# Performance work log

Hardware: AMD Instinct MI355X
Metric: run time of the kernel (lower is better)

## Reference

```python
import jax, jax.numpy as jnp
from jax import lax
import numpy as np

GAMMA, WARP = 0.01, 134.4          # SoftDTW(gamma=0.01, warp=134.4)
INF, BIG = 100000.0, 1e9           # INF from kl_loss_sdtw; BIG ~ math.inf boundary
KL_A, KL_FWD_A, GEN_A, GEN_E2E_A, FEAT_A, DUR_A, MEL_A = 1.0, 1.0, 1.0, 1.0, 1.0, 1.0, 45.0


def soft_dtw(D):
    """Soft-DTW with warp penalty. D: [B, N, M] -> R[:, N, M].
    R[i,j] = D[i-1,j-1] + softmin_gamma(R[i-1,j-1], R[i-1,j]+warp, R[i,j-1]+warp)."""
    B, N, M = D.shape
    row0 = jnp.full((B, M + 1), BIG, D.dtype).at[:, 0].set(0.0)  # R[0, :]

    def row_step(prev_row, d_row):                 # prev_row: [B, M+1], d_row: [B, M]
        left0 = jnp.full((B,), BIG, D.dtype)       # R[i, 0]

        def col_step(r_left, inp):
            d, r_diag, r_up = inp                  # each [B]
            r0 = -r_diag / GAMMA
            r1 = -(r_up + WARP) / GAMMA
            r2 = -(r_left + WARP) / GAMMA
            rmax = jnp.maximum(jnp.maximum(r0, r1), r2)
            smin = -GAMMA * (jnp.log(jnp.exp(r0 - rmax) + jnp.exp(r1 - rmax) + jnp.exp(r2 - rmax)) + rmax)
            r = d + smin
            return r, r

        xs = (d_row.T, prev_row[:, :-1].T, prev_row[:, 1:].T)   # scan over j=1..M
        _, vals = lax.scan(col_step, left0, xs)                 # [M, B]
        new_row = jnp.concatenate([left0[:, None], vals.T], axis=1)
        return new_row, None

    last, _ = lax.scan(row_step, row0, jnp.swapaxes(D, 0, 1))   # scan over i=1..N
    return last[:, M]


def sdtw_kl_matrix(z, logs_q, m, logs_p):
    """kl[b,i,j] = sum_h logs_p - logs_q - 0.5 + 0.5*(z-m)^2*exp(-2 logs_p).
    m, logs_p: [b,h,tp]; z, logs_q: [b,h,tq] -> [b,tp,tq] via 3 batched GEMMs."""
    h = m.shape[1]
    w = jnp.exp(-2.0 * logs_p)                                   # [b,h,tp]
    quad = (jnp.einsum('bhi,bhj->bij', w, z * z)
            - 2.0 * jnp.einsum('bhi,bhj->bij', w * m, z)
            + jnp.sum(w * m * m, axis=1)[:, :, None])
    return (jnp.sum(logs_p, axis=1)[:, :, None]
            - jnp.sum(logs_q, axis=1)[:, None, :]
            - 0.5 * h + 0.5 * quad)


def kl_loss_sdtw(z, logs_q, m, logs_p, p_mask, q_mask):
    kl = sdtw_kl_matrix(z, logs_q, m, logs_p)
    kl = jnp.pad(kl, ((0, 0), (0, 1), (0, 1)))
    pm = jnp.pad(p_mask, ((0, 0), (0, 1)))
    qm = jnp.pad(q_mask, ((0, 0), (0, 1)))
    pb = pm[:, :, None].astype(bool)
    qb = qm[:, None, :].astype(bool)
    kl = jnp.where(pb ^ qb, INF, kl)
    kl = jnp.where((~pb) & (~qb), 0.0, kl)
    return jnp.sum(soft_dtw(kl)) / jnp.sum(pm)


def _forward(mel_slice, mel_slice_hat, scores_disc_fake, scores_disc_fake_e2e,
             feats_disc_real, feats_disc_fake, loss_duration, loss_duration_len,
             loss_pitch, z_p, m_p, logs_p, z_q, m_q, logs_q, p_mask, z_mask):
    # generator losses: sum over discriminators of mean((1-score)^2)
    loss_gen = jnp.sum(jnp.mean((1.0 - scores_disc_fake) ** 2, axis=(1, 2))) * GEN_A
    loss_gen_e2e = jnp.sum(jnp.mean((1.0 - scores_disc_fake_e2e) ** 2, axis=(1, 2))) * GEN_E2E_A
    # feature-matching loss (real feats detached)
    fr = lax.stop_gradient(feats_disc_real)
    loss_fm = jnp.sum(jnp.mean(jnp.abs(fr - feats_disc_fake), axis=(1, 2, 3))) * 2.0 * FEAT_A
    loss_mel = jnp.mean(jnp.abs(mel_slice - mel_slice_hat)) * MEL_A
    loss_dur = jnp.sum(loss_duration) * DUR_A
    loss_dur_len = jnp.log(loss_duration_len + 1e-6)
    zm = z_mask[:, 0, :]
    loss_kl = kl_loss_sdtw(z_p, logs_q, m_p, logs_p, p_mask, zm) * KL_A
    loss_kl_fwd = kl_loss_sdtw(z_q, logs_p, m_q, logs_q, zm, p_mask) * KL_FWD_A
    return (loss_gen + loss_gen_e2e + loss_fm + loss_mel + loss_dur
            + loss_dur_len + loss_kl + loss_kl_fwd)


def setup_inputs() -> dict:
    key = jax.random.key(0)
    ks = jax.random.split(key, 16)
    B, H, TP, TQ = 4, 192, 350, 400
    return {
        'mel_slice': jax.random.normal(ks[0], (B, 80, 128), jnp.float32),
        'mel_slice_hat': jax.random.normal(ks[1], (B, 80, 128), jnp.float32),
        'scores_disc_fake': jax.random.normal(ks[2], (6, B, 8192), jnp.float32),
        'scores_disc_fake_e2e': jax.random.normal(ks[3], (6, B, 8192), jnp.float32),
        'feats_disc_real': jax.random.normal(ks[4], (24, B, 128, 4096), jnp.float32),
        'feats_disc_fake': jax.random.normal(ks[5], (24, B, 128, 4096), jnp.float32),
        'loss_duration': jax.random.uniform(ks[6], (B, TP), jnp.float32) * 0.01,
        'loss_duration_len': jax.random.uniform(ks[7], (), jnp.float32) + 0.5,
        'loss_pitch': jax.random.uniform(ks[8], (B, TP), jnp.float32),
        'z_p': jax.random.normal(ks[9], (B, H, TQ), jnp.float32),
        'm_p': jax.random.normal(ks[10], (B, H, TP), jnp.float32),
        'logs_p': 0.1 * jax.random.normal(ks[11], (B, H, TP), jnp.float32),
        'z_q': jax.random.normal(ks[12], (B, H, TP), jnp.float32),
        'm_q': jax.random.normal(ks[13], (B, H, TQ), jnp.float32),
        'logs_q': 0.1 * jax.random.normal(ks[14], (B, H, TQ), jnp.float32),
        'p_mask': jnp.ones((B, TP), jnp.float32),
        'z_mask': jnp.ones((B, 1, TQ), jnp.float32),
    }


def reference(mel_slice, mel_slice_hat, scores_disc_fake, scores_disc_fake_e2e,
              feats_disc_real, feats_disc_fake, loss_duration, loss_duration_len,
              loss_pitch, z_p, m_p, logs_p, z_q, m_q, logs_q, p_mask, z_mask):
    return _forward(mel_slice, mel_slice_hat, scores_disc_fake, scores_disc_fake_e2e,
                    feats_disc_real, feats_disc_fake, loss_duration, loss_duration_len,
                    loss_pitch, z_p, m_p, logs_p, z_q, m_q, logs_q, p_mask, z_mask)
```

## Files before the change

### kernel.cpp

```cpp
#include <hip/hip_runtime.h>
#include <math.h>

#define GAMMA_ 0.01f
#define WARP_  134.4f
#define INFV   100000.0f
#define BIGV   1000000000.0f

#define B_  4
#define H_  192
#define TP_ 350
#define TQ_ 400

#define ACC_OFF 0
#define DTW_OFF 16
#define SLP_OFF 32
#define SLQ_OFF (SLP_OFF + B_*TP_)
#define KL1_OFF 3072
#define KL1_NCOL 401
#define KL1_PITCHT 352
#define KL2_OFF (KL1_OFF + B_*KL1_NCOL*KL1_PITCHT)
#define KL2_NCOL 351
#define KL2_PITCHT 408

#define RING_SLOTS 67
#define RING_PITCH 416

typedef float f4_t __attribute__((ext_vector_type(4)));

__device__ __forceinline__ unsigned pk2(float a, float b) {
    unsigned ua = __float_as_uint(a), ub = __float_as_uint(b);
    ua = (ua + 0x7FFFu + ((ua >> 16) & 1u)) >> 16;
    ub = (ub + 0x7FFFu + ((ub >> 16) & 1u)) & 0xFFFF0000u;
    return ua | ub;
}

__global__ void sl_kernel(const float* __restrict__ logs_p,
                          const float* __restrict__ logs_q,
                          float* __restrict__ ws) {
    int t = blockIdx.x * 256 + threadIdx.x;
    if (t < 32) ws[ACC_OFF + t] = 0.f;
    if (t < B_ * TP_) {
        int b = t / TP_, i = t % TP_;
        const float* p = logs_p + (size_t)b * H_ * TP_ + i;
        float s = 0.f;
        for (int h = 0; h < H_; ++h) s += p[(size_t)h * TP_];
        ws[SLP_OFF + t] = s;
    } else if (t < B_ * TP_ + B_ * TQ_) {
        int t2 = t - B_ * TP_;
        int b = t2 / TQ_, j = t2 % TQ_;
        const float* p = logs_q + (size_t)b * H_ * TQ_ + j;
        float s = 0.f;
        for (int h = 0; h < H_; ++h) s += p[(size_t)h * TQ_];
        ws[SLQ_OFF + t2] = s;
    }
}

__global__ void kl_kernel(const float* __restrict__ mp, const float* __restrict__ lsp,
                          const float* __restrict__ zp,
                          const float* __restrict__ mq, const float* __restrict__ lsq,
                          const float* __restrict__ zq,
                          const float* __restrict__ pmask, const float* __restrict__ zmask,
                          float* __restrict__ ws) {
    int which = blockIdx.z >> 2;
    int b     = blockIdx.z & 3;
    const float *mS, *lS, *zS, *SLrow, *SLcol, *rm, *cm; float* out; int R, C, pitchT;
    if (which == 0) { mS=mp; lS=lsp; zS=zp; SLrow=ws+SLP_OFF; SLcol=ws+SLQ_OFF;
                      rm=pmask + b*TP_; cm=zmask + b*TQ_;
                      out=ws+KL1_OFF + (size_t)b*KL1_NCOL*KL1_PITCHT;
                      R=TP_; C=TQ_; pitchT=KL1_PITCHT; }
    else            { mS=mq; lS=lsq; zS=zq; SLrow=ws+SLQ_OFF; SLcol=ws+SLP_OFF;
                      rm=zmask + b*TQ_; cm=pmask + b*TP_;
                      out=ws+KL2_OFF + (size_t)b*KL2_NCOL*KL2_PITCHT;
                      R=TQ_; C=TP_; pitchT=KL2_PITCHT; }
    int i0 = blockIdx.x * 32;
    int j0 = blockIdx.y * 32;
    if (i0 > R || j0 > C) return;
    __shared__ __align__(16) float wS [16][32];
    __shared__ __align__(16) float mSh[16][32];
    __shared__ __align__(16) float zSh[16][32];
    const float* mB = mS + (size_t)b * H_ * R;
    const float* lB = lS + (size_t)b * H_ * R;
    const float* zB = zS + (size_t)b * H_ * C;
    int tx = threadIdx.x, ty = threadIdx.y;
    int t  = ty * 16 + tx;
    float a00 = 0.f, a01 = 0.f, a10 = 0.f, a11 = 0.f;
    for (int h0 = 0; h0 < H_; h0 += 16) {
        for (int e = t; e < 512; e += 256) {
            int hh = e >> 5, cc = e & 31;
            int h = h0 + hh;
            int gi = i0 + cc, gj = j0 + cc;
            float wv = 0.f, mv = 0.f;
            if (gi < R) {
                wv = __expf(-2.f * lB[(size_t)h * R + gi]);
                mv = mB[(size_t)h * R + gi];
            }
            wS[hh][cc] = wv; mSh[hh][cc] = mv;
            zSh[hh][cc] = (gj < C) ? zB[(size_t)h * C + gj] : 0.f;
        }
        __syncthreads();
#pragma unroll
        for (int kk = 0; kk < 16; ++kk) {
            float2 wv = *(const float2*)&wS [kk][tx * 2];
            float2 mv = *(const float2*)&mSh[kk][tx * 2];
            float2 zv = *(const float2*)&zSh[kk][ty * 2];
            float d;
            d = zv.x - mv.x; a00 += wv.x * d * d;
            d = zv.x - mv.y; a01 += wv.y * d * d;
            d = zv.y - mv.x; a10 += wv.x * d * d;
            d = zv.y - mv.y; a11 += wv.y * d * d;
        }
        __syncthreads();
    }
    float accs[2][2] = {{a00, a01}, {a10, a11}};
    for (int jj = 0; jj < 2; ++jj)
        for (int ii = 0; ii < 2; ++ii) {
            int I = i0 + tx * 2 + ii, J = j0 + ty * 2 + jj;
            if (I <= R && J <= C) {
                bool pbI = (I < R) && (rm[I] != 0.f);
                bool qbJ = (J < C) && (cm[J] != 0.f);
                float v;
                if (pbI & qbJ)
                    v = SLrow[b * R + I] - SLcol[b * C + J] - 0.5f * H_ + 0.5f * accs[jj][ii];
                else
                    v = (pbI ^ qbJ) ? INFV : 0.f;
                out[(size_t)J * pitchT + I] = v;
            }
        }
}

#define SLD(q, r, cc, ii, vv) { int col_ = ((q) << 3) + (cc); \
    if ((vv) && col_ <= C_) r = *(const f4_t*)(klT + (size_t)col_ * pitchT + ((ii) << 2)); }
#define SST(q, r, cc, ii, vv) { int col_ = ((q) << 3) + (cc); \
    if ((vv) && col_ <= C_) { int s_ = col_ - (col_ / RING_SLOTS) * RING_SLOTS; \
        uint2 u_; u_.x = pk2(r.x, r.y); u_.y = pk2(r.z, r.w); \
        *(uint2*)&ring[s_][(ii) << 2] = u_; } }

__global__ __launch_bounds__(512, 1) void main_kernel(
    const float* __restrict__ mel, const float* __restrict__ melh,
    const float* __restrict__ sg,  const float* __restrict__ se,
    const float* __restrict__ fr,  const float* __restrict__ ff,
    const float* __restrict__ dur, float* ws) {
    __shared__ __align__(16) unsigned short ring[RING_SLOTS + 2][RING_PITCH];
    __shared__ float sbuf[64];
    int bid = blockIdx.x, tid = threadIdx.x;
    if (bid < 8) {
        int b = bid & 3, which = bid >> 2;
        int R_, C_, pitchT;
        const float* klT;
        if (which == 0) {
            R_ = TP_; C_ = TQ_; pitchT = KL1_PITCHT;
            klT = ws + KL1_OFF + (size_t)b * KL1_NCOL * KL1_PITCHT;
        } else {
            R_ = TQ_; C_ = TP_; pitchT = KL2_PITCHT;
            klT = ws + KL2_OFF + (size_t)b * KL2_NCOL * KL2_PITCHT;
        }
        int lres = R_ >> 3;
        int kres = R_ & 7;
        int tmax = C_ + lres;
        int P = (tmax + 8) >> 3;

        if (tid < 64) {
            int lane = tid; bool lane0 = (lane == 0);
            float p0=BIGV,p1=BIGV,p2=BIGV,p3=BIGV,p4=BIGV,p5=BIGV,p6=BIGV,p7=BIGV;
            float recv_cur = BIGV, recv_prev = BIGV;
            __syncthreads();
            for (int p = 0; p < P; ++p) {
                int t0 = p << 3;
                int c0 = t0 - lane;
                int cr = c0 < 0 ? 0 : (c0 > C_ ? C_ : c0);
                int s0 = cr - (cr / RING_SLOTS) * RING_SLOTS;
                int4 rd = *(const int4*)&ring[s0][lane << 3];
#pragma unroll
                for (int i = 0; i < 8; ++i) {
                    int c = t0 + i - lane;
                    int4 ru = rd;
                    if (i < 7) {
                        int cn = c + 1; cn = cn < 0 ? 0 : (cn > C_ ? C_ : cn);
                        int sn = cn - (cn / RING_SLOTS) * RING_SLOTS;
                        rd = *(const int4*)&ring[sn][lane << 3];
                    }
                    float last_ = 0.f;
                    if ((unsigned)c <= (unsigned)C_) {
                        float u_  = lane0 ? BIGV : recv_cur;
                        float dg_ = (c == 0) ? (lane0 ? 0.f : BIGV) : (lane0 ? BIGV : recv_prev);
                        float d0 = __uint_as_float((unsigned)ru.x << 16);
                        float d1 = __uint_as_float((unsigned)ru.x & 0xFFFF0000u);
                        float d2 = __uint_as_float((unsigned)ru.y << 16);
                        float d3 = __uint_as_float((unsigned)ru.y & 0xFFFF0000u);
                        float d4 = __uint_as_float((unsigned)ru.z << 16);
                        float d5 = __uint_as_float((unsigned)ru.z & 0xFFFF0000u);
                        float d6 = __uint_as_float((unsigned)ru.w << 16);
                        float d7 = __uint_as_float((unsigned)ru.w & 0xFFFF0000u);
                        float B0 = WARP_ + d0, B1 = WARP_ + d1, B2 = WARP_ + d2, B3 = WARP_ + d3;
                        float B4 = WARP_ + d4, B5 = WARP_ + d5, B6 = WARP_ + d6, B7 = WARP_ + d7;
                        float P0 = fminf(dg_ + d0, p0 + B0);
                        float P1 = fminf(p0 + d1, p1 + B1);
                        float P2 = fminf(p1 + d2, p2 + B2);
                        float P3 = fminf(p2 + d3, p3 + B3);
                        float P4 = fminf(p3 + d4, p4 + B4);
                        float P5 = fminf(p4 + d5, p5 + B5);
                        float P6 = fminf(p5 + d6, p6 + B6);
                        float P7 = fminf(p6 + d7, p7 + B7);
                        u_ = fminf(P0, u_ + B0); p0 = u_;
                        u_ = fminf(P1, u_ + B1); p1 = u_;
                        u_ = fminf(P2, u_ + B2); p2 = u_;
                        u_ = fminf(P3, u_ + B3); p3 = u_;
                        u_ = fminf(P4, u_ + B4); p4 = u_;
                        u_ = fminf(P5, u_ + B5); p5 = u_;
                        u_ = fminf(P6, u_ + B6); p6 = u_;
                        u_ = fminf(P7, u_ + B7); p7 = u_;
                        last_ = u_;
                    }
                    recv_prev = recv_cur;
                    recv_cur  = __shfl_up(last_, 1);
                }
                __syncthreads();
            }
            float q0 = __shfl(p0, lres), q1 = __shfl(p1, lres), q2 = __shfl(p2, lres),
                  q3 = __shfl(p3, lres), q4 = __shfl(p4, lres), q5 = __shfl(p5, lres),
                  q6 = __shfl(p6, lres), q7 = __shfl(p7, lres);
            if (lane0) {
                float res = (kres == 0) ? q0 : (kres == 1) ? q1 : (kres == 2) ? q2 :
                            (kres == 3) ? q3 : (kres == 4) ? q4 : (kres == 5) ? q5 :
                            (kres == 6) ? q6 : q7;
                ws[DTW_OFF + which * 4 + b] = res;
            }
        } else {
            int st  = tid - 64;
            int n4  = pitchT >> 2;
            int tot = n4 << 3;
            int cA = st / n4,  iA = st - cA * n4;
            int eB = st + 448; int cB = eB / n4, iB = eB - cB * n4;
            bool vA = st < tot, vB = eB < tot;
            f4_t rA = {0.f,0.f,0.f,0.f}, rB = {0.f,0.f,0.f,0.f};
            SLD(0, rA, cA, iA, vA) SLD(0, rB, cB, iB, vB)
            SST(0, rA, cA, iA, vA) SST(0, rB, cB, iB, vB)
            SLD(1, rA, cA, iA, vA) SLD(1, rB, cB, iB, vB)
            __syncthreads();
            for (int p = 0; p < P; ++p) {
                SST(p + 1, rA, cA, iA, vA) SST(p + 1, rB, cB, iB, vB)
                SLD(p + 2, rA, cA, iA, vA) SLD(p + 2, rB, cB, iB, vB)
                __syncthreads();
            }
        }
    } else {
        int rid = bid - 8;
        long NR = (long)gridDim.x - 8;
        const float4* fr4   = (const float4*)fr;
        const float4* ff4   = (const float4*)ff;
        const float4* sg4   = (const float4*)sg;
        const float4* se4   = (const float4*)se;
        const float4* mel4  = (const float4*)mel;
        const float4* melh4 = (const float4*)melh;
        const float4* dur4  = (const float4*)dur;
        const long E0 = 12582912;
        const long E1 = E0 + 49152;
        const long E2 = E1 + 49152;
        const long E3 = E2 + 10240;
        const long E4 = E3 + 350;
        float a0=0.f,a1=0.f,a2=0.f,a3=0.f,a4=0.f;
        long stride = NR * 512;
        for (long v = (long)rid * 512 + tid; v < E4; v += stride) {
            if (v < E0) {
                float4 x = fr4[v], y = ff4[v];
                a2 += fabsf(x.x - y.x) + fabsf(x.y - y.y) + fabsf(x.z - y.z) + fabsf(x.w - y.w);
            } else if (v < E1) {
                float4 s = sg4[v - E0]; float e;
                e = 1.f - s.x; a0 += e * e; e = 1.f - s.y; a0 += e * e;
                e = 1.f - s.z; a0 += e * e; e = 1.f - s.w; a0 += e * e;
            } else if (v < E2) {
                float4 s = se4[v - E1]; float e;
                e = 1.f - s.x; a1 += e * e; e = 1.f - s.y; a1 += e * e;
                e = 1.f - s.z; a1 += e * e; e = 1.f - s.w; a1 += e * e;
            } else if (v < E3) {
                float4 x = mel4[v - E2], y = melh4[v - E2];
                a3 += fabsf(x.x - y.x) + fabsf(x.y - y.y) + fabsf(x.z - y.z) + fabsf(x.w - y.w);
            } else {
                float4 x = dur4[v - E3]; a4 += x.x + x.y + x.z + x.w;
            }
        }
        float vals[5] = {a0, a1, a2, a3, a4};
#pragma unroll
        for (int q = 0; q < 5; ++q) {
            float v = vals[q];
            for (int off = 32; off > 0; off >>= 1) v += __shfl_xor(v, off);
            if ((tid & 63) == 0) sbuf[(tid >> 6) * 8 + q] = v;
        }
        __syncthreads();
        if (tid < 5) {
            float s = 0.f;
            for (int w = 0; w < 8; ++w) s += sbuf[w * 8 + tid];
            atomicAdd(&ws[ACC_OFF + tid], s);
        }
    }
}

__global__ void masksum_kernel(const float* __restrict__ pmask,
                               const float* __restrict__ zmask,
                               float* __restrict__ ws) {
    int tid = threadIdx.x;
    float a5 = 0.f, a6 = 0.f;
    for (int v = tid; v < B_ * TP_; v += 256) a5 += pmask[v];
    for (int v = tid; v < B_ * TQ_; v += 256) a6 += zmask[v];
    __shared__ float s5[4], s6[4];
    for (int off = 32; off > 0; off >>= 1) { a5 += __shfl_xor(a5, off); a6 += __shfl_xor(a6, off); }
    if ((tid & 63) == 0) { s5[tid >> 6] = a5; s6[tid >> 6] = a6; }
    __syncthreads();
    if (tid == 0) {
        ws[5] = s5[0] + s5[1] + s5[2] + s5[3];
        ws[6] = s6[0] + s6[1] + s6[2] + s6[3];
    }
}

__global__ void final_kernel(const float* __restrict__ ws,
                             const float* __restrict__ ldl,
                             float* __restrict__ out) {
    if (threadIdx.x == 0 && blockIdx.x == 0) {
        float gen  = ws[0] * (1.f / 32768.f);
        float e2e  = ws[1] * (1.f / 32768.f);
        float fm   = ws[2] * (2.f / 2097152.f);
        float melv = ws[3] * (45.f / 40960.f);
        float durv = ws[4];
        float dlen = logf(ldl[0] + 1e-6f);
        float kl  = (ws[DTW_OFF + 0] + ws[DTW_OFF + 1] + ws[DTW_OFF + 2] + ws[DTW_OFF + 3]) / ws[5];
        float klf = (ws[DTW_OFF + 4] + ws[DTW_OFF + 5] + ws[DTW_OFF + 6] + ws[DTW_OFF + 7]) / ws[6];
        out[0] = gen + e2e + fm + melv + durv + dlen + kl + klf;
    }
}

extern "C" void kernel_launch(void* const* d_in, const int* in_sizes, int n_in,
                              void* d_out, int out_size, void* d_ws, size_t ws_size,
                              hipStream_t stream) {
    const float* mel    = (const float*)d_in[0];
    const float* melh   = (const float*)d_in[1];
    const float* sg     = (const float*)d_in[2];
    const float* se     = (const float*)d_in[3];
    const float* fr     = (const float*)d_in[4];
    const float* ff     = (const float*)d_in[5];
    const float* dur    = (const float*)d_in[6];
    const float* ldl    = (const float*)d_in[7];
    const float* z_p    = (const float*)d_in[9];
    const float* m_p    = (const float*)d_in[10];
    const float* logs_p = (const float*)d_in[11];
    const float* z_q    = (const float*)d_in[12];
    const float* m_q    = (const float*)d_in[13];
    const float* logs_q = (const float*)d_in[14];
    const float* pmask  = (const float*)d_in[15];
    const float* zmask  = (const float*)d_in[16];
    float* ws  = (float*)d_ws;
    float* out = (float*)d_out;

    sl_kernel<<<12, 256, 0, stream>>>(logs_p, logs_q, ws);
    masksum_kernel<<<1, 256, 0, stream>>>(pmask, zmask, ws);
    kl_kernel<<<dim3(13, 13, 8), dim3(16, 16), 0, stream>>>(
        m_p, logs_p, z_p, m_q, logs_q, z_q, pmask, zmask, ws);
    main_kernel<<<8 + 1016, 512, 0, stream>>>(mel, melh, sg, se, fr, ff, dur, ws);
    final_kernel<<<1, 64, 0, stream>>>(ws, ldl, out);
}
```

Before: 166.9 us.

## Widen DTW wavefront to 16 rows per lane and shrink LDS ring for occupancy

The DTW wavefront now gives each lane 16 rows instead of 8, so only about 26 lanes cover the rows and the serial phase count shrinks by roughly half the lane-diagonal length. The ring buffer is cut from 67 to 43 slots and the separate reduction buffer reuses the ring, which lowers LDS use so launch bounds can allow 4 blocks per CU for the reduction blocks. The reduction path is split: the large feature L1 sum gets a 2x-unrolled grid-stride loop, and the small tensors are handled with one load per thread. Risks are more register pressure per lane in the DTW loop, and a hardcoded row-residue selection (p14 vs p0) that only holds for these exact sizes.

```diff
diff --git a/kernel.cpp b/kernel.cpp
--- a/kernel.cpp
+++ b/kernel.cpp
@@ -22,7 +22,7 @@
 #define KL2_NCOL 351
 #define KL2_PITCHT 408
 
-#define RING_SLOTS 67
+#define RING_SLOTS 43
 #define RING_PITCH 416
 
 typedef float f4_t __attribute__((ext_vector_type(4)));
@@ -33,6 +33,7 @@
     ub = (ub + 0x7FFFu + ((ub >> 16) & 1u)) & 0xFFFF0000u;
     return ua | ub;
 }
+__device__ __forceinline__ int mod43(int x) { return x - (x / RING_SLOTS) * RING_SLOTS; }
 
 __global__ void sl_kernel(const float* __restrict__ logs_p,
                           const float* __restrict__ logs_q,
@@ -131,17 +132,22 @@
 #define SLD(q, r, cc, ii, vv) { int col_ = ((q) << 3) + (cc); \
     if ((vv) && col_ <= C_) r = *(const f4_t*)(klT + (size_t)col_ * pitchT + ((ii) << 2)); }
 #define SST(q, r, cc, ii, vv) { int col_ = ((q) << 3) + (cc); \
-    if ((vv) && col_ <= C_) { int s_ = col_ - (col_ / RING_SLOTS) * RING_SLOTS; \
+    if ((vv) && col_ <= C_) { int s_ = mod43(col_); \
         uint2 u_; u_.x = pk2(r.x, r.y); u_.y = pk2(r.z, r.w); \
         *(uint2*)&ring[s_][(ii) << 2] = u_; } }
 
-__global__ __launch_bounds__(512, 1) void main_kernel(
+#define UNPK(da, db, src) \
+    float da = __uint_as_float((unsigned)(src) << 16); \
+    float db = __uint_as_float((unsigned)(src) & 0xFFFF0000u);
+#define PRE(k, km1) float q##k = fminf(p##km1 + d##k, p##k + (WARP_ + d##k));
+#define CH(k) u_ = fminf(q##k, u_ + (WARP_ + d##k)); p##k = u_;
+
+__global__ __launch_bounds__(512, 4) void main_kernel(
     const float* __restrict__ mel, const float* __restrict__ melh,
     const float* __restrict__ sg,  const float* __restrict__ se,
     const float* __restrict__ fr,  const float* __restrict__ ff,
     const float* __restrict__ dur, float* ws) {
-    __shared__ __align__(16) unsigned short ring[RING_SLOTS + 2][RING_PITCH];
-    __shared__ float sbuf[64];
+    __shared__ __align__(16) unsigned short ring[RING_SLOTS][RING_PITCH];
     int bid = blockIdx.x, tid = threadIdx.x;
     if (bid < 8) {
         int b = bid & 3, which = bid >> 2;
@@ -154,61 +160,49 @@
             R_ = TQ_; C_ = TP_; pitchT = KL2_PITCHT;
             klT = ws + KL2_OFF + (size_t)b * KL2_NCOL * KL2_PITCHT;
         }
-        int lres = R_ >> 3;
-        int kres = R_ & 7;
+        int lres = R_ >> 4;
         int tmax = C_ + lres;
-        int P = (tmax + 8) >> 3;
+        int P = (tmax >> 3) + 1;
 
         if (tid < 64) {
             int lane = tid; bool lane0 = (lane == 0);
-            float p0=BIGV,p1=BIGV,p2=BIGV,p3=BIGV,p4=BIGV,p5=BIGV,p6=BIGV,p7=BIGV;
+            int lnOff = (lane < 26 ? lane : 25) << 4;
+            float p0=BIGV,p1=BIGV,p2=BIGV,p3=BIGV,p4=BIGV,p5=BIGV,p6=BIGV,p7=BIGV,
+                  p8=BIGV,p9=BIGV,p10=BIGV,p11=BIGV,p12=BIGV,p13=BIGV,p14=BIGV,p15=BIGV;
             float recv_cur = BIGV, recv_prev = BIGV;
             __syncthreads();
-            for (int p = 0; p < P; ++p) {
-                int t0 = p << 3;
+            for (int ph = 0; ph < P; ++ph) {
+                int t0 = ph << 3;
                 int c0 = t0 - lane;
                 int cr = c0 < 0 ? 0 : (c0 > C_ ? C_ : c0);
-                int s0 = cr - (cr / RING_SLOTS) * RING_SLOTS;
-                int4 rd = *(const int4*)&ring[s0][lane << 3];
+                int s0 = mod43(cr);
+                int4 n0 = *(const int4*)&ring[s0][lnOff];
+                int4 n1 = *(const int4*)&ring[s0][lnOff + 8];
 #pragma unroll
                 for (int i = 0; i < 8; ++i) {
                     int c = t0 + i - lane;
-                    int4 ru = rd;
+                    int4 r0 = n0, r1 = n1;
                     if (i < 7) {
                         int cn = c + 1; cn = cn < 0 ? 0 : (cn > C_ ? C_ : cn);
-                        int sn = cn - (cn / RING_SLOTS) * RING_SLOTS;
-                        rd = *(const int4*)&ring[sn][lane << 3];
+                        int sn = mod43(cn);
+                        n0 = *(const int4*)&ring[sn][lnOff];
+                        n1 = *(const int4*)&ring[sn][lnOff + 8];
                     }
                     float last_ = 0.f;
                     if ((unsigned)c <= (unsigned)C_) {
                         float u_  = lane0 ? BIGV : recv_cur;
-                        float dg_ = (c == 0) ? (lane0 ? 0.f : BIGV) : (lane0 ? BIGV : recv_prev);
-                        float d0 = __uint_as_float((unsigned)ru.x << 16);
-                        float d1 = __uint_as_float((unsigned)ru.x & 0xFFFF0000u);
-                        float d2 = __uint_as_float((unsigned)ru.y << 16);
-                        float d3 = __uint_as_float((unsigned)ru.y & 0xFFFF0000u);
-                        float d4 = __uint_as_float((unsigned)ru.z << 16);
-                        float d5 = __uint_as_float((unsigned)ru.z & 0xFFFF0000u);
-                        float d6 = __uint_as_float((unsigned)ru.w << 16);
-                        float d7 = __uint_as_float((unsigned)ru.w & 0xFFFF0000u);
-                        float B0 = WARP_ + d0, B1 = WARP_ + d1, B2 = WARP_ + d2, B3 = WARP_ + d3;
-                        float B4 = WARP_ + d4, B5 = WARP_ + d5, B6 = WARP_ + d6, B7 = WARP_ + d7;
-                        float P0 = fminf(dg_ + d0, p0 + B0);
-                        float P1 = fminf(p0 + d1, p1 + B1);
-                        float P2 = fminf(p1 + d2, p2 + B2);
-                        float P3 = fminf(p2 + d3, p3 + B3);
-                        float P4 = fminf(p3 + d4, p4 + B4);
-                        float P5 = fminf(p4 + d5, p5 + B5);
-                        float P6 = fminf(p5 + d6, p6 + B6);
-                        float P7 = fminf(p6 + d7, p7 + B7);
-                        u_ = fminf(P0, u_ + B0); p0 = u_;
-                        u_ = fminf(P1, u_ + B1); p1 = u_;
-                        u_ = fminf(P2, u_ + B2); p2 = u_;
-                        u_ = fminf(P3, u_ + B3); p3 = u_;
-                        u_ = fminf(P4, u_ + B4); p4 = u_;
-                        u_ = fminf(P5, u_ + B5); p5 = u_;
-                        u_ = fminf(P6, u_ + B6); p6 = u_;
-                        u_ = fminf(P7, u_ + B7); p7 = u_;
+                        float dg  = (c == 0) ? (lane0 ? 0.f : BIGV) : (lane0 ? BIGV : recv_prev);
+                        UNPK(d0,  d1,  r0.x) UNPK(d2,  d3,  r0.y)
+                        UNPK(d4,  d5,  r0.z) UNPK(d6,  d7,  r0.w)
+                        UNPK(d8,  d9,  r1.x) UNPK(d10, d11, r1.y)
+                        UNPK(d12, d13, r1.z) UNPK(d14, d15, r1.w)
+                        float q0 = fminf(dg + d0, p0 + (WARP_ + d0));
+                        PRE(1,0)  PRE(2,1)   PRE(3,2)   PRE(4,3)
+                        PRE(5,4)  PRE(6,5)   PRE(7,6)   PRE(8,7)
+                        PRE(9,8)  PRE(10,9)  PRE(11,10) PRE(12,11)
+                        PRE(13,12) PRE(14,13) PRE(15,14)
+                        CH(0) CH(1) CH(2) CH(3) CH(4) CH(5) CH(6) CH(7)
+                        CH(8) CH(9) CH(10) CH(11) CH(12) CH(13) CH(14) CH(15)
                         last_ = u_;
                     }
                     recv_prev = recv_cur;
@@ -216,15 +210,9 @@
                 }
                 __syncthreads();
             }
-            float q0 = __shfl(p0, lres), q1 = __shfl(p1, lres), q2 = __shfl(p2, lres),
-                  q3 = __shfl(p3, lres), q4 = __shfl(p4, lres), q5 = __shfl(p5, lres),
-                  q6 = __shfl(p6, lres), q7 = __shfl(p7, lres);
-            if (lane0) {
-                float res = (kres == 0) ? q0 : (kres == 1) ? q1 : (kres == 2) ? q2 :
-                            (kres == 3) ? q3 : (kres == 4) ? q4 : (kres == 5) ? q5 :
-                            (kres == 6) ? q6 : q7;
-                ws[DTW_OFF + which * 4 + b] = res;
-            }
+            float r14 = __shfl(p14, lres);
+            float r0x = __shfl(p0,  lres);
+            if (lane0) ws[DTW_OFF + which * 4 + b] = (which == 0) ? r14 : r0x;
         } else {
             int st  = tid - 64;
             int n4  = pitchT >> 2;
@@ -245,7 +233,8 @@
         }
     } else {
         int rid = bid - 8;
-        long NR = (long)gridDim.x - 8;
+        long T = (long)(gridDim.x - 8) * 512;
+        long gid = (long)rid * 512 + tid;
         const float4* fr4   = (const float4*)fr;
         const float4* ff4   = (const float4*)ff;
         const float4* sg4   = (const float4*)sg;
@@ -254,42 +243,46 @@
         const float4* melh4 = (const float4*)melh;
         const float4* dur4  = (const float4*)dur;
         const long E0 = 12582912;
-        const long E1 = E0 + 49152;
-        const long E2 = E1 + 49152;
-        const long E3 = E2 + 10240;
-        const long E4 = E3 + 350;
-        float a0=0.f,a1=0.f,a2=0.f,a3=0.f,a4=0.f;
-        long stride = NR * 512;
-        for (long v = (long)rid * 512 + tid; v < E4; v += stride) {
-            if (v < E0) {
-                float4 x = fr4[v], y = ff4[v];
-                a2 += fabsf(x.x - y.x) + fabsf(x.y - y.y) + fabsf(x.z - y.z) + fabsf(x.w - y.w);
-            } else if (v < E1) {
-                float4 s = sg4[v - E0]; float e;
-                e = 1.f - s.x; a0 += e * e; e = 1.f - s.y; a0 += e * e;
-                e = 1.f - s.z; a0 += e * e; e = 1.f - s.w; a0 += e * e;
-            } else if (v < E2) {
-                float4 s = se4[v - E1]; float e;
-                e = 1.f - s.x; a1 += e * e; e = 1.f - s.y; a1 += e * e;
-                e = 1.f - s.z; a1 += e * e; e = 1.f - s.w; a1 += e * e;
-            } else if (v < E3) {
-                float4 x = mel4[v - E2], y = melh4[v - E2];
-                a3 += fabsf(x.x - y.x) + fabsf(x.y - y.y) + fabsf(x.z - y.z) + fabsf(x.w - y.w);
+        float a2 = 0.f;
+        long v = gid;
+        for (; v + T < E0; v += 2 * T) {
+            float4 x0 = fr4[v],     y0 = ff4[v];
+            float4 x1 = fr4[v + T], y1 = ff4[v + T];
+            a2 += fabsf(x0.x-y0.x)+fabsf(x0.y-y0.y)+fabsf(x0.z-y0.z)+fabsf(x0.w-y0.w);
+            a2 += fabsf(x1.x-y1.x)+fabsf(x1.y-y1.y)+fabsf(x1.z-y1.z)+fabsf(x1.w-y1.w);
+        }
+        for (; v < E0; v += T) {
+            float4 x = fr4[v], y = ff4[v];
+            a2 += fabsf(x.x-y.x)+fabsf(x.y-y.y)+fabsf(x.z-y.z)+fabsf(x.w-y.w);
+        }
+        float a0=0.f, a1=0.f, a3=0.f, a4=0.f;
+        long w = gid;
+        if (w < 108894) {
+            if (w < 49152) {
+                float4 s = sg4[w]; float e;
+                e=1.f-s.x; a0+=e*e; e=1.f-s.y; a0+=e*e; e=1.f-s.z; a0+=e*e; e=1.f-s.w; a0+=e*e;
+            } else if (w < 98304) {
+                float4 s = se4[w - 49152]; float e;
+                e=1.f-s.x; a1+=e*e; e=1.f-s.y; a1+=e*e; e=1.f-s.z; a1+=e*e; e=1.f-s.w; a1+=e*e;
+            } else if (w < 108544) {
+                float4 x = mel4[w - 98304], y = melh4[w - 98304];
+                a3 += fabsf(x.x-y.x)+fabsf(x.y-y.y)+fabsf(x.z-y.z)+fabsf(x.w-y.w);
             } else {
-                float4 x = dur4[v - E3]; a4 += x.x + x.y + x.z + x.w;
+                float4 x = dur4[w - 108544]; a4 += x.x + x.y + x.z + x.w;
             }
         }
         float vals[5] = {a0, a1, a2, a3, a4};
+        float* sb = (float*)ring;
 #pragma unroll
         for (int q = 0; q < 5; ++q) {
-            float v = vals[q];
-            for (int off = 32; off > 0; off >>= 1) v += __shfl_xor(v, off);
-            if ((tid & 63) == 0) sbuf[(tid >> 6) * 8 + q] = v;
+            float x = vals[q];
+            for (int off = 32; off > 0; off >>= 1) x += __shfl_xor(x, off);
+            if ((tid & 63) == 0) sb[(tid >> 6) * 8 + q] = x;
         }
         __syncthreads();
         if (tid < 5) {
             float s = 0.f;
-            for (int w = 0; w < 8; ++w) s += sbuf[w * 8 + tid];
+            for (int w2 = 0; w2 < 8; ++w2) s += sb[w2 * 8 + tid];
             atomicAdd(&ws[ACC_OFF + tid], s);
         }
     }
```

Measured after the change: 196.0 us. +17.4%, slower.

## Deepen stager prefetch, use raw LDS barrier, and unroll reduction loop

Applied to the files above, without the earlier changes.

The staging warps in the DTW blocks now keep four register buffers and issue global loads for four future column groups every fourth phase, so there are more loads in flight ahead of the ring-buffer stores. The per-phase __syncthreads is replaced by an explicit lgkmcnt wait plus s_barrier, so vmem loads stay outstanding across the barrier. The reduction blocks split the big feature-L1 stream into a 2x-unrolled loop and handle the small tensors in a single branch-free pass, reusing the ring LDS as scratch. This uses more registers and the code relies on assumptions about the thread counts covering the small tensors.

```diff
diff --git a/kernel.cpp b/kernel.cpp
--- a/kernel.cpp
+++ b/kernel.cpp
@@ -33,6 +33,7 @@
     ub = (ub + 0x7FFFu + ((ub >> 16) & 1u)) & 0xFFFF0000u;
     return ua | ub;
 }
+__device__ __forceinline__ int modS(int x) { return x - (x / RING_SLOTS) * RING_SLOTS; }
 
 __global__ void sl_kernel(const float* __restrict__ logs_p,
                           const float* __restrict__ logs_q,
@@ -128,12 +129,23 @@
         }
 }
 
-#define SLD(q, r, cc, ii, vv) { int col_ = ((q) << 3) + (cc); \
-    if ((vv) && col_ <= C_) r = *(const f4_t*)(klT + (size_t)col_ * pitchT + ((ii) << 2)); }
-#define SST(q, r, cc, ii, vv) { int col_ = ((q) << 3) + (cc); \
-    if ((vv) && col_ <= C_) { int s_ = col_ - (col_ / RING_SLOTS) * RING_SLOTS; \
-        uint2 u_; u_.x = pk2(r.x, r.y); u_.y = pk2(r.z, r.w); \
-        *(uint2*)&ring[s_][(ii) << 2] = u_; } }
+#define SLD2(BK, q) { int col_; \
+    col_ = ((q) << 3) + cA; \
+    if (vA && col_ <= C_) rA##BK = *(const f4_t*)(klT + (size_t)col_ * pitchT + (iA << 2)); \
+    col_ = ((q) << 3) + cB; \
+    if (vB && col_ <= C_) rB##BK = *(const f4_t*)(klT + (size_t)col_ * pitchT + (iB << 2)); }
+#define SST2(BK, q) { int col_; \
+    col_ = ((q) << 3) + cA; \
+    if (vA && col_ <= C_) { int s_ = modS(col_); \
+        uint2 u_; u_.x = pk2(rA##BK.x, rA##BK.y); u_.y = pk2(rA##BK.z, rA##BK.w); \
+        *(uint2*)&ring[s_][iA << 2] = u_; } \
+    col_ = ((q) << 3) + cB; \
+    if (vB && col_ <= C_) { int s_ = modS(col_); \
+        uint2 u_; u_.x = pk2(rB##BK.x, rB##BK.y); u_.y = pk2(rB##BK.z, rB##BK.w); \
+        *(uint2*)&ring[s_][iB << 2] = u_; } }
+
+#define STAGER_BAR() { asm volatile("s_waitcnt lgkmcnt(0)" ::: "memory"); \
+                       __builtin_amdgcn_s_barrier(); }
 
 __global__ __launch_bounds__(512, 1) void main_kernel(
     const float* __restrict__ mel, const float* __restrict__ melh,
@@ -141,7 +153,6 @@
     const float* __restrict__ fr,  const float* __restrict__ ff,
     const float* __restrict__ dur, float* ws) {
     __shared__ __align__(16) unsigned short ring[RING_SLOTS + 2][RING_PITCH];
-    __shared__ float sbuf[64];
     int bid = blockIdx.x, tid = threadIdx.x;
     if (bid < 8) {
         int b = bid & 3, which = bid >> 2;
@@ -157,18 +168,18 @@
         int lres = R_ >> 3;
         int kres = R_ & 7;
         int tmax = C_ + lres;
-        int P = (tmax + 8) >> 3;
+        int P = (tmax >> 3) + 1;
 
         if (tid < 64) {
             int lane = tid; bool lane0 = (lane == 0);
             float p0=BIGV,p1=BIGV,p2=BIGV,p3=BIGV,p4=BIGV,p5=BIGV,p6=BIGV,p7=BIGV;
             float recv_cur = BIGV, recv_prev = BIGV;
             __syncthreads();
-            for (int p = 0; p < P; ++p) {
-                int t0 = p << 3;
+            for (int ph = 0; ph < P; ++ph) {
+                int t0 = ph << 3;
                 int c0 = t0 - lane;
                 int cr = c0 < 0 ? 0 : (c0 > C_ ? C_ : c0);
-                int s0 = cr - (cr / RING_SLOTS) * RING_SLOTS;
+                int s0 = modS(cr);
                 int4 rd = *(const int4*)&ring[s0][lane << 3];
 #pragma unroll
                 for (int i = 0; i < 8; ++i) {
@@ -176,13 +187,13 @@
                     int4 ru = rd;
                     if (i < 7) {
                         int cn = c + 1; cn = cn < 0 ? 0 : (cn > C_ ? C_ : cn);
-                        int sn = cn - (cn / RING_SLOTS) * RING_SLOTS;
+                        int sn = modS(cn);
                         rd = *(const int4*)&ring[sn][lane << 3];
                     }
                     float last_ = 0.f;
                     if ((unsigned)c <= (unsigned)C_) {
                         float u_  = lane0 ? BIGV : recv_cur;
-                        float dg_ = (c == 0) ? (lane0 ? 0.f : BIGV) : (lane0 ? BIGV : recv_prev);
+                        float dg  = (c == 0) ? (lane0 ? 0.f : BIGV) : (lane0 ? BIGV : recv_prev);
                         float d0 = __uint_as_float((unsigned)ru.x << 16);
                         float d1 = __uint_as_float((unsigned)ru.x & 0xFFFF0000u);
                         float d2 = __uint_as_float((unsigned)ru.y << 16);
@@ -193,7 +204,7 @@
                         float d7 = __uint_as_float((unsigned)ru.w & 0xFFFF0000u);
                         float B0 = WARP_ + d0, B1 = WARP_ + d1, B2 = WARP_ + d2, B3 = WARP_ + d3;
                         float B4 = WARP_ + d4, B5 = WARP_ + d5, B6 = WARP_ + d6, B7 = WARP_ + d7;
-                        float P0 = fminf(dg_ + d0, p0 + B0);
+                        float P0 = fminf(dg + d0, p0 + B0);
                         float P1 = fminf(p0 + d1, p1 + B1);
                         float P2 = fminf(p1 + d2, p2 + B2);
                         float P3 = fminf(p2 + d3, p3 + B3);
@@ -232,20 +243,29 @@
             int cA = st / n4,  iA = st - cA * n4;
             int eB = st + 448; int cB = eB / n4, iB = eB - cB * n4;
             bool vA = st < tot, vB = eB < tot;
-            f4_t rA = {0.f,0.f,0.f,0.f}, rB = {0.f,0.f,0.f,0.f};
-            SLD(0, rA, cA, iA, vA) SLD(0, rB, cB, iB, vB)
-            SST(0, rA, cA, iA, vA) SST(0, rB, cB, iB, vB)
-            SLD(1, rA, cA, iA, vA) SLD(1, rB, cB, iB, vB)
-            __syncthreads();
+            f4_t rA0={0,0,0,0}, rA1={0,0,0,0}, rA2={0,0,0,0}, rA3={0,0,0,0};
+            f4_t rB0={0,0,0,0}, rB1={0,0,0,0}, rB2={0,0,0,0}, rB3={0,0,0,0};
+            SLD2(0, 0)
+            SST2(0, 0)
+            SLD2(1, 1)
+            STAGER_BAR();
             for (int p = 0; p < P; ++p) {
-                SST(p + 1, rA, cA, iA, vA) SST(p + 1, rB, cB, iB, vB)
-                SLD(p + 2, rA, cA, iA, vA) SLD(p + 2, rB, cB, iB, vB)
-                __syncthreads();
+                switch ((p + 1) & 3) {
+                    case 0: SST2(0, p + 1) break;
+                    case 1: SST2(1, p + 1) break;
+                    case 2: SST2(2, p + 1) break;
+                    default: SST2(3, p + 1) break;
+                }
+                if ((p & 3) == 0) {
+                    SLD2(2, p + 2) SLD2(3, p + 3) SLD2(0, p + 4) SLD2(1, p + 5)
+                }
+                STAGER_BAR();
             }
         }
     } else {
         int rid = bid - 8;
-        long NR = (long)gridDim.x - 8;
+        long T = (long)(gridDim.x - 8) * 512;
+        long gid = (long)rid * 512 + tid;
         const float4* fr4   = (const float4*)fr;
         const float4* ff4   = (const float4*)ff;
         const float4* sg4   = (const float4*)sg;
@@ -254,42 +274,46 @@
         const float4* melh4 = (const float4*)melh;
         const float4* dur4  = (const float4*)dur;
         const long E0 = 12582912;
-        const long E1 = E0 + 49152;
-        const long E2 = E1 + 49152;
-        const long E3 = E2 + 10240;
-        const long E4 = E3 + 350;
-        float a0=0.f,a1=0.f,a2=0.f,a3=0.f,a4=0.f;
-        long stride = NR * 512;
-        for (long v = (long)rid * 512 + tid; v < E4; v += stride) {
-            if (v < E0) {
-                float4 x = fr4[v], y = ff4[v];
-                a2 += fabsf(x.x - y.x) + fabsf(x.y - y.y) + fabsf(x.z - y.z) + fabsf(x.w - y.w);
-            } else if (v < E1) {
-                float4 s = sg4[v - E0]; float e;
-                e = 1.f - s.x; a0 += e * e; e = 1.f - s.y; a0 += e * e;
-                e = 1.f - s.z; a0 += e * e; e = 1.f - s.w; a0 += e * e;
-            } else if (v < E2) {
-                float4 s = se4[v - E1]; float e;
-                e = 1.f - s.x; a1 += e * e; e = 1.f - s.y; a1 += e * e;
-                e = 1.f - s.z; a1 += e * e; e = 1.f - s.w; a1 += e * e;
-            } else if (v < E3) {
-                float4 x = mel4[v - E2], y = melh4[v - E2];
-                a3 += fabsf(x.x - y.x) + fabsf(x.y - y.y) + fabsf(x.z - y.z) + fabsf(x.w - y.w);
+        float a2 = 0.f;
+        long v = gid;
+        for (; v + T < E0; v += 2 * T) {
+            float4 x0 = fr4[v],     y0 = ff4[v];
+            float4 x1 = fr4[v + T], y1 = ff4[v + T];
+            a2 += fabsf(x0.x-y0.x)+fabsf(x0.y-y0.y)+fabsf(x0.z-y0.z)+fabsf(x0.w-y0.w);
+            a2 += fabsf(x1.x-y1.x)+fabsf(x1.y-y1.y)+fabsf(x1.z-y1.z)+fabsf(x1.w-y1.w);
+        }
+        for (; v < E0; v += T) {
+            float4 x = fr4[v], y = ff4[v];
+            a2 += fabsf(x.x-y.x)+fabsf(x.y-y.y)+fabsf(x.z-y.z)+fabsf(x.w-y.w);
+        }
+        float a0=0.f, a1=0.f, a3=0.f, a4=0.f;
+        long w = gid;
+        if (w < 108894) {
+            if (w < 49152) {
+                float4 s = sg4[w]; float e;
+                e=1.f-s.x; a0+=e*e; e=1.f-s.y; a0+=e*e; e=1.f-s.z; a0+=e*e; e=1.f-s.w; a0+=e*e;
+            } else if (w < 98304) {
+                float4 s = se4[w - 49152]; float e;
+                e=1.f-s.x; a1+=e*e; e=1.f-s.y; a1+=e*e; e=1.f-s.z; a1+=e*e; e=1.f-s.w; a1+=e*e;
+            } else if (w < 108544) {
+                float4 x = mel4[w - 98304], y = melh4[w - 98304];
+                a3 += fabsf(x.x-y.x)+fabsf(x.y-y.y)+fabsf(x.z-y.z)+fabsf(x.w-y.w);
             } else {
-                float4 x = dur4[v - E3]; a4 += x.x + x.y + x.z + x.w;
+                float4 x = dur4[w - 108544]; a4 += x.x + x.y + x.z + x.w;
             }
         }
         float vals[5] = {a0, a1, a2, a3, a4};
+        float* sb = (float*)ring;
 #pragma unroll
         for (int q = 0; q < 5; ++q) {
-            float v = vals[q];
-            for (int off = 32; off > 0; off >>= 1) v += __shfl_xor(v, off);
-            if ((tid & 63) == 0) sbuf[(tid >> 6) * 8 + q] = v;
+            float x = vals[q];
+            for (int off = 32; off > 0; off >>= 1) x += __shfl_xor(x, off);
+            if ((tid & 63) == 0) sb[(tid >> 6) * 8 + q] = x;
         }
         __syncthreads();
         if (tid < 5) {
             float s = 0.f;
-            for (int w = 0; w < 8; ++w) s += sbuf[w * 8 + tid];
+            for (int w2 = 0; w2 < 8; ++w2) s += sb[w2 * 8 + tid];
             atomicAdd(&ws[ACC_OFF + tid], s);
         }
     }
```

Measured after the change: 200.5 us. 1.2x slower.
